# Optimization experiments

Measured on AMD Instinct MI355X. Metric: run time of the kernel, lower is better.

The kernel has to match this reference:

```python
import jax, jax.numpy as jnp
import numpy as np

N, E, H, L, R, NG = 8192, 131072, 256, 3, 128, 64
NUM_ELEMENTS = 80
CUTOFF = 12.0
INV_SQRT_2 = 1.0 / np.sqrt(2.0)
INV_SQRT_3 = 1.0 / np.sqrt(3.0)
INV_SQRT_H = 1.0 / np.sqrt(H)


def _glorot(key, shape):
    fan_in, fan_out = shape[-2], shape[-1]
    return jax.random.normal(key, shape, jnp.float32) * np.sqrt(2.0 / (fan_in + fan_out))


def setup_inputs():
    key = jax.random.key(0)
    ks = jax.random.split(key, 24)
    pos = jax.random.normal(ks[0], (N, 3), jnp.float32) * 5.0
    z = jax.random.randint(ks[1], (N,), 0, NUM_ELEMENTS)
    src = jax.random.randint(ks[2], (E,), 0, N)
    off = jax.random.randint(ks[3], (E,), 1, N)
    dst = (src + off) % N  # guarantee no self-loops (dist > 0)
    edge_index = jnp.stack([src, dst])
    batch = jnp.sort(jax.random.randint(ks[4], (N,), 0, NG))
    return {
        "pos": pos,
        "atom_emb": jax.random.normal(ks[5], (NUM_ELEMENTS, H), jnp.float32),
        "ln_w": jnp.ones((L, H), jnp.float32),
        "ln_b": jnp.zeros((L, H), jnp.float32),
        "xp_w1": _glorot(ks[6], (L, H, H)),
        "xp_b1": jnp.zeros((L, H), jnp.float32),
        "xp_w2": _glorot(ks[7], (L, H, 3 * H)),
        "xp_b2": jnp.zeros((L, 3 * H), jnp.float32),
        "rbf_w": _glorot(ks[8], (L, R, 3 * H)),
        "rbf_b": jnp.zeros((L, 3 * H), jnp.float32),
        "vec_w": _glorot(ks[9], (L, H, 2 * H)),
        "xv_w1": _glorot(ks[10], (L, 2 * H, H)),
        "xv_b1": jnp.zeros((L, H), jnp.float32),
        "xv_w2": _glorot(ks[11], (L, H, 3 * H)),
        "xv_b2": jnp.zeros((L, 3 * H), jnp.float32),
        "oe_w1": _glorot(ks[12], (H, H // 2)),
        "oe_b1": jnp.zeros((H // 2,), jnp.float32),
        "oe_w2": _glorot(ks[13], (H // 2, 1)),
        "oe_b2": jnp.zeros((1,), jnp.float32),
        "z": z,
        "edge_index": edge_index,
        "batch": batch,
    }


def _gaussian_rbf(dist):
    offset = jnp.linspace(0.0, CUTOFF, R)
    coeff = -0.5 / (offset[1] - offset[0]) ** 2
    return jnp.exp(coeff * (dist[:, None] - offset[None, :]) ** 2)  # [E, R]


def _layernorm(x, w, b):
    mu = x.mean(-1, keepdims=True)
    var = x.var(-1, keepdims=True)
    return (x - mu) / jnp.sqrt(var + 1e-5) * w + b


def reference(pos, atom_emb, ln_w, ln_b, xp_w1, xp_b1, xp_w2, xp_b2,
              rbf_w, rbf_b, vec_w, xv_w1, xv_b1, xv_w2, xv_b2,
              oe_w1, oe_b1, oe_w2, oe_b2, z, edge_index, batch):
    src, dst = edge_index[0], edge_index[1]
    rel = pos[src] - pos[dst]                       # [E, 3]
    dist = jnp.sqrt((rel ** 2).sum(-1))             # [E]
    edge_rbf = _gaussian_rbf(dist)                  # [E, R]
    edge_vector = rel / dist[:, None]               # [E, 3] unit vectors

    x = atom_emb[z]                                 # [N, H]
    vec = jnp.zeros((N, 3, H), x.dtype)

    for l in range(L):
        # ---- PaiNNMessage ----
        xh = _layernorm(x, ln_w[l], ln_b[l])
        xh = jax.nn.silu(xh @ xp_w1[l] + xp_b1[l]) @ xp_w2[l] + xp_b2[l]  # [N, 3H]
        rbfh = edge_rbf @ rbf_w[l] + rbf_b[l]                             # [E, 3H]
        m = xh[src] * rbfh
        mx, xh2, xh3 = jnp.split(m, 3, axis=-1)
        xh2 = xh2 * INV_SQRT_3
        mvec = (vec[src] * xh2[:, None, :] + xh3[:, None, :] * edge_vector[:, :, None]) * INV_SQRT_H
        dx = jax.ops.segment_sum(mx, dst, num_segments=N)
        dvec = jax.ops.segment_sum(mvec, dst, num_segments=N)
        x = (x + dx) * INV_SQRT_2
        vec = vec + dvec

        # ---- PaiNNUpdate ----
        vp = vec @ vec_w[l]                          # [N, 3, 2H]
        vec1, vec2 = jnp.split(vp, 2, axis=-1)
        vec_dot = (vec1 * vec2).sum(axis=1) * INV_SQRT_H           # [N, H]
        vnorm = jnp.sqrt((vec2 ** 2).sum(axis=1) + 1e-8)           # [N, H]
        h = jnp.concatenate([x, vnorm], axis=-1)
        h = jax.nn.silu(h @ xv_w1[l] + xv_b1[l]) @ xv_w2[l] + xv_b2[l]
        xv1, xv2, xv3 = jnp.split(h, 3, axis=-1)
        dx = (xv1 + xv2 * vec_dot) * INV_SQRT_2
        dvec = xv3[:, None, :] * vec1
        x = (x + dx) * INV_SQRT_2
        vec = vec + dvec

    # ---- energy head: per-atom MLP then per-molecule sum ----
    per_atom = jax.nn.silu(x @ oe_w1 + oe_b1) @ oe_w2 + oe_b2      # [N, 1]
    energy = jax.ops.segment_sum(per_atom, batch, num_segments=NG)  # [NG, 1]
    return energy
```

## Files before the change

### kernel.cpp

```cpp
#include <hip/hip_runtime.h>
#include <hip/hip_bf16.h>
#include <math.h>

#define NN 8192
#define EE 131072
#define HH 256
#define LL 3
#define RR 128
#define NGG 64
#define MSG_WAVES 16

typedef __attribute__((ext_vector_type(8))) short bf16x8;
typedef __attribute__((ext_vector_type(4))) float f32x4;
typedef unsigned short u16;

union U4 { ushort4 v; unsigned short a[4]; };
union U8 { uint4 v; unsigned short a[8]; };

__device__ __forceinline__ float silu(float v) { return v / (1.0f + expf(-v)); }
__device__ __forceinline__ float b2f(unsigned short u) { return __uint_as_float(((unsigned)u) << 16); }
__device__ __forceinline__ unsigned short f2b(float f) {
    unsigned u = __float_as_uint(f);
    u += 0x7fff + ((u >> 16) & 1);
    return (unsigned short)(u >> 16);
}

constexpr float kInvSqrt2 = 0.70710678118654752440f;
constexpr float kInvSqrt3 = 0.57735026918962576451f;
constexpr float kInvSqrtH = 0.0625f;

__global__ void k_zero(float* __restrict__ p, int n4) {
    int i = blockIdx.x * 256 + threadIdx.x;
    if (i < n4) ((float4*)p)[i] = make_float4(0.f, 0.f, 0.f, 0.f);
}

__global__ __launch_bounds__(256) void k_wt_all(
    const float* __restrict__ xp_w1, const float* __restrict__ xp_w2,
    const float* __restrict__ rbf_w, const float* __restrict__ vec_w,
    const float* __restrict__ xv_w1, const float* __restrict__ xv_w2,
    const float* __restrict__ oe_w1,
    u16* __restrict__ xp_w1T, u16* __restrict__ xp_w2T, u16* __restrict__ rbf_wKb,
    u16* __restrict__ vec_wT, u16* __restrict__ xv_w1T, u16* __restrict__ xv_w2T,
    u16* __restrict__ oe_w1T) {
    int bid = blockIdx.x;
    const float* src; u16* dst; int K, N, t, cast = 0;
    if (bid < 2400) {
        int l = bid / 800, r = bid % 800;
        if (r < 64)       { src = xp_w1 + (size_t)l * 65536;  dst = xp_w1T + (size_t)l * 65536;  K = 256; N = 256; t = r; }
        else if (r < 256) { src = xp_w2 + (size_t)l * 196608; dst = xp_w2T + (size_t)l * 196608; K = 256; N = 768; t = r - 64; }
        else if (r < 352) { src = rbf_w + (size_t)l * 98304;  dst = rbf_wKb + (size_t)l * 98304; K = 128; N = 768; t = r - 256; cast = 1; }
        else if (r < 480) { src = vec_w + (size_t)l * 131072; dst = vec_wT + (size_t)l * 131072; K = 256; N = 512; t = r - 352; }
        else if (r < 608) { src = xv_w1 + (size_t)l * 131072; dst = xv_w1T + (size_t)l * 131072; K = 512; N = 256; t = r - 480; }
        else              { src = xv_w2 + (size_t)l * 196608; dst = xv_w2T + (size_t)l * 196608; K = 256; N = 768; t = r - 608; }
    } else {
        src = oe_w1; dst = oe_w1T; K = 256; N = 128; t = bid - 2400;
    }
    int nx = N >> 5;
    int bn = (t % nx) * 32, bk = (t / nx) * 32;
    int tx = threadIdx.x & 31, ty = threadIdx.x >> 5;
    if (cast) {
#pragma unroll
        for (int i = 0; i < 32; i += 8)
            dst[(size_t)(bk + ty + i) * N + bn + tx] = f2b(src[(size_t)(bk + ty + i) * N + bn + tx]);
        return;
    }
    __shared__ float tile[32][33];
#pragma unroll
    for (int i = 0; i < 32; i += 8)
        tile[ty + i][tx] = src[(size_t)(bk + ty + i) * N + bn + tx];
    __syncthreads();
#pragma unroll
    for (int i = 0; i < 32; i += 8)
        dst[(size_t)(bn + ty + i) * K + bk + tx] = f2b(tile[tx][ty + i]);
}

__global__ void k_init_ln(const float* __restrict__ emb, const int* __restrict__ z,
                          const float* __restrict__ w, const float* __restrict__ b,
                          float* __restrict__ x, u16* __restrict__ xlnb) {
    int n = blockIdx.x, t = threadIdx.x;
    float v = emb[z[n] * HH + t];
    x[(size_t)n * HH + t] = v;
    float s = v, q = v * v;
#pragma unroll
    for (int m = 32; m >= 1; m >>= 1) {
        s += __shfl_xor(s, m, 64);
        q += __shfl_xor(q, m, 64);
    }
    __shared__ float s_sum[4], s_sq[4];
    int wid = t >> 6;
    if ((t & 63) == 0) { s_sum[wid] = s; s_sq[wid] = q; }
    __syncthreads();
    float S = s_sum[0] + s_sum[1] + s_sum[2] + s_sum[3];
    float Q = s_sq[0] + s_sq[1] + s_sq[2] + s_sq[3];
    float mu = S * (1.0f / HH);
    float var = Q * (1.0f / HH) - mu * mu;
    float rs = rsqrtf(var + 1e-5f);
    xlnb[(size_t)n * HH + t] = f2b((v - mu) * rs * w[t] + b[t]);
}

__global__ void k_geom_hist(const float* __restrict__ pos, const int* __restrict__ ei,
                            float* __restrict__ ev, int* __restrict__ deg) {
    int e = blockIdx.x * 256 + threadIdx.x;
    if (e >= EE) return;
    int s = ei[e], d = ei[EE + e];
    float rx = pos[s * 3 + 0] - pos[d * 3 + 0];
    float ry = pos[s * 3 + 1] - pos[d * 3 + 1];
    float rz = pos[s * 3 + 2] - pos[d * 3 + 2];
    float dist = sqrtf(rx * rx + ry * ry + rz * rz);
    float inv = 1.0f / dist;
    ((float4*)ev)[e] = make_float4(rx * inv, ry * inv, rz * inv, dist);
    atomicAdd(&deg[d], 1);
}

__global__ void k_scan_sort(const int* __restrict__ deg, int* __restrict__ row_ptr,
                            int* __restrict__ fill, int* __restrict__ dorder) {
    __shared__ int buf[256];
    __shared__ int carry_s;
    int t = threadIdx.x;
    if (t == 0) carry_s = 0;
    __syncthreads();
    for (int r = 0; r < NN; r += 256) {
        int v = deg[r + t];
        buf[t] = v;
        __syncthreads();
        for (int ofs = 1; ofs < 256; ofs <<= 1) {
            int add = (t >= ofs) ? buf[t - ofs] : 0;
            __syncthreads();
            buf[t] += add;
            __syncthreads();
        }
        int excl = buf[t] - v;
        int carry = carry_s;
        row_ptr[r + t] = carry + excl;
        fill[r + t] = carry + excl;
        __syncthreads();
        if (t == 255) carry_s = carry + buf[t];
        __syncthreads();
    }
    if (t == 0) row_ptr[NN] = carry_s;
    __syncthreads();
    __shared__ int bins[256];
    __shared__ int base[256];
    bins[t] = 0;
    __syncthreads();
    for (int d = t; d < NN; d += 256) {
        int b = deg[d]; b = b > 255 ? 255 : b;
        atomicAdd(&bins[b], 1);
    }
    __syncthreads();
    if (t == 0) {
        int acc = 0;
        for (int k = 255; k >= 0; --k) { base[k] = acc; acc += bins[k]; }
    }
    __syncthreads();
    bins[t] = 0;
    __syncthreads();
    for (int d = t; d < NN; d += 256) {
        int b = deg[d]; b = b > 255 ? 255 : b;
        int p = atomicAdd(&bins[b], 1);
        dorder[base[b] + p] = d;
    }
}

__global__ void k_scatter(const int* __restrict__ ei, const float* __restrict__ ev,
                          int* __restrict__ fill, int* __restrict__ srcp,
                          float4* __restrict__ evp, int* __restrict__ k0tab,
                          float* __restrict__ gtab) {
    int e = blockIdx.x * 256 + threadIdx.x;
    if (e >= EE) return;
    int d = ei[EE + e];
    int pos = atomicAdd(&fill[d], 1);
    float4 e4 = ((const float4*)ev)[e];
    srcp[pos] = ei[e];
    evp[pos] = e4;
    const float step = 12.0f / 127.0f;
    const float coeff = -0.5f / (step * step);
    float dist = e4.w;
    int k0 = (int)floorf(dist / step) - 3;
    k0 = k0 < 0 ? 0 : (k0 > 120 ? 120 : k0);
    float g[8];
#pragma unroll
    for (int k = 0; k < 8; ++k) {
        float t = dist - (k0 + k) * step;
        g[k] = expf(coeff * t * t);
    }
    k0tab[pos] = k0;
    ((float4*)gtab)[pos * 2 + 0] = make_float4(g[0], g[1], g[2], g[3]);
    ((float4*)gtab)[pos * 2 + 1] = make_float4(g[4], g[5], g[6], g[7]);
}

template <int AF32, int OUT_BF16, int ACT>
__global__ __launch_bounds__(256) void k_gemm(
    const void* __restrict__ Av, const u16* __restrict__ BT,
    const float* __restrict__ bias, void* __restrict__ C, int M, int K, int N) {
    __shared__ uint4 As4[512];
    __shared__ uint4 Bs4[512];
    u16* As = (u16*)As4;
    u16* Bs = (u16*)Bs4;
    int tid = threadIdx.x;
    int wave = tid >> 6, lane = tid & 63;
    int bm = blockIdx.y * 128, bn = blockIdx.x * 128;
    int wm = (wave >> 1) * 64, wn = (wave & 1) * 64;
    int lm = lane & 15;
    int kg = lane >> 4;
    f32x4 acc[4][4] = {};

    for (int k0 = 0; k0 < K; k0 += 32) {
#pragma unroll
        for (int it = 0; it < 2; ++it) {
            int idx = it * 256 + tid;
            int r = idx >> 2, seg = idx & 3;
            if (AF32) {
                const float* Af = (const float*)Av;
                float4 fa = *(const float4*)&Af[(size_t)(bm + r) * K + k0 + seg * 8];
                float4 fb = *(const float4*)&Af[(size_t)(bm + r) * K + k0 + seg * 8 + 4];
                U8 u;
                u.a[0] = f2b(fa.x); u.a[1] = f2b(fa.y); u.a[2] = f2b(fa.z); u.a[3] = f2b(fa.w);
                u.a[4] = f2b(fb.x); u.a[5] = f2b(fb.y); u.a[6] = f2b(fb.z); u.a[7] = f2b(fb.w);
                As4[idx] = u.v;
            } else {
                const u16* A = (const u16*)Av;
                As4[idx] = *(const uint4*)&A[(size_t)(bm + r) * K + k0 + seg * 8];
            }
            Bs4[idx] = *(const uint4*)&BT[(size_t)(bn + r) * K + k0 + seg * 8];
        }
        __syncthreads();
        bf16x8 af[4], bfr[4];
#pragma unroll
        for (int i = 0; i < 4; ++i)
            af[i] = *(const bf16x8*)&As[(wm + i * 16 + lm) * 32 + kg * 8];
#pragma unroll
        for (int j = 0; j < 4; ++j)
            bfr[j] = *(const bf16x8*)&Bs[(wn + j * 16 + lm) * 32 + kg * 8];
#pragma unroll
        for (int i = 0; i < 4; ++i)
#pragma unroll
            for (int j = 0; j < 4; ++j)
                acc[i][j] = __builtin_amdgcn_mfma_f32_16x16x32_bf16(af[i], bfr[j], acc[i][j], 0, 0, 0);
        __syncthreads();
    }

#pragma unroll
    for (int j = 0; j < 4; ++j) {
        int col = bn + wn + j * 16 + lm;
        float bv = bias ? bias[col] : 0.f;
#pragma unroll
        for (int i = 0; i < 4; ++i) {
            int row0 = bm + wm + i * 16 + kg * 4;
#pragma unroll
            for (int r = 0; r < 4; ++r) {
                float v = acc[i][j][r] + bv;
                if (ACT) v = silu(v);
                if (OUT_BF16)
                    ((u16*)C)[(size_t)(row0 + r) * N + col] = f2b(v);
                else
                    ((float*)C)[(size_t)(row0 + r) * N + col] = v;
            }
        }
    }
}

__global__ __launch_bounds__(1024) void k_msg(
    const u16* __restrict__ xhb, const u16* __restrict__ vinb,
    const int* __restrict__ srcp, const float4* __restrict__ evp,
    const int* __restrict__ row_ptr, const int* __restrict__ k0tab,
    const float* __restrict__ gtab, const u16* __restrict__ WK ,
    const float* __restrict__ rbias, float* __restrict__ x,
    const float* __restrict__ vin, float* __restrict__ vecM,
    const int* __restrict__ dorder) {
    __shared__ u16 Wp[128 * 256];
    int tid = threadIdx.x;
    int wave = tid >> 6, lane = tid & 63;
    int c0 = lane * 4;
    int blk = blockIdx.x;
    int band = (blk < 256) ? blk : (767 - blk);
    int d = dorder[band * MSG_WAVES + wave];
    int E0 = row_ptr[d], E1 = row_ptr[d + 1];
    float accv[3][4] = {};

#pragma unroll
    for (int p = 0; p < 3; ++p) {
        __syncthreads();
#pragma unroll
        for (int it = 0; it < 4; ++it) {
            int idx = it * 1024 + tid;
            int row = idx >> 5;
            int col8 = (idx & 31) * 8;
            *(uint4*)&Wp[row * 256 + col8] =
                *(const uint4*)&WK[(size_t)row * 768 + p * 256 + col8];
        }
        __syncthreads();
        float4 bb = ((const float4*)(rbias + p * 256))[lane];
        float bias4[4] = {bb.x, bb.y, bb.z, bb.w};
        float accx[4] = {};
        for (int j = E0; j < E1; ++j) {
            int s = srcp[j];
            int kj = k0tab[j];
            float4 ga = ((const float4*)gtab)[(size_t)j * 2 + 0];
            float4 gb = ((const float4*)gtab)[(size_t)j * 2 + 1];
            float g[8] = {ga.x, ga.y, ga.z, ga.w, gb.x, gb.y, gb.z, gb.w};
            float rr[4] = {bias4[0], bias4[1], bias4[2], bias4[3]};
#pragma unroll
            for (int k = 0; k < 8; ++k) {
                U4 w;
                w.v = *(const ushort4*)&Wp[(kj + k) * 256 + c0];
#pragma unroll
                for (int c = 0; c < 4; ++c) rr[c] += g[k] * b2f(w.a[c]);
            }
            if (p == 0) {
                U4 X; X.v = *(const ushort4*)(xhb + (size_t)s * 768 + c0);
#pragma unroll
                for (int c = 0; c < 4; ++c) accx[c] += b2f(X.a[c]) * rr[c];
            } else if (p == 1) {
                U4 X, V0, V1, V2;
                X.v = *(const ushort4*)(xhb + (size_t)s * 768 + 256 + c0);
                V0.v = *(const ushort4*)(vinb + (size_t)s * 768 + c0);
                V1.v = *(const ushort4*)(vinb + (size_t)s * 768 + 256 + c0);
                V2.v = *(const ushort4*)(vinb + (size_t)s * 768 + 512 + c0);
#pragma unroll
                for (int c = 0; c < 4; ++c) {
                    float m1 = b2f(X.a[c]) * rr[c] * kInvSqrt3;
                    accv[0][c] += b2f(V0.a[c]) * m1;
                    accv[1][c] += b2f(V1.a[c]) * m1;
                    accv[2][c] += b2f(V2.a[c]) * m1;
                }
            } else {
                U4 X; X.v = *(const ushort4*)(xhb + (size_t)s * 768 + 512 + c0);
                float4 ev4 = evp[j];
#pragma unroll
                for (int c = 0; c < 4; ++c) {
                    float m2 = b2f(X.a[c]) * rr[c];
                    accv[0][c] += m2 * ev4.x;
                    accv[1][c] += m2 * ev4.y;
                    accv[2][c] += m2 * ev4.z;
                }
            }
        }
        if (p == 0) {
            size_t xi = (size_t)d * 256 + c0;
            float4 xv = *(const float4*)&x[xi];
            xv.x = (xv.x + accx[0]) * kInvSqrt2;
            xv.y = (xv.y + accx[1]) * kInvSqrt2;
            xv.z = (xv.z + accx[2]) * kInvSqrt2;
            xv.w = (xv.w + accx[3]) * kInvSqrt2;
            *(float4*)&x[xi] = xv;
        }
    }
#pragma unroll
    for (int k = 0; k < 3; ++k) {
        size_t idx = (size_t)d * 768 + k * 256 + c0;
        float4 vv = *(const float4*)&vin[idx];
        vv.x += accv[k][0] * kInvSqrtH;
        vv.y += accv[k][1] * kInvSqrtH;
        vv.z += accv[k][2] * kInvSqrtH;
        vv.w += accv[k][3] * kInvSqrtH;
        *(float4*)&vecM[idx] = vv;
    }
}

__global__ void k_vecdot(const u16* __restrict__ vp, const float* __restrict__ x,
                         float* __restrict__ vec_dot, u16* __restrict__ hcat) {
    int i = blockIdx.x * 256 + threadIdx.x;
    int n = i >> 8, c = i & 255;
    const u16* p = vp + (size_t)n * 1536;
    float dsum = 0.f, qsum = 0.f;
#pragma unroll
    for (int k = 0; k < 3; ++k) {
        float v1 = b2f(p[k * 512 + c]);
        float v2 = b2f(p[k * 512 + 256 + c]);
        dsum += v1 * v2;
        qsum += v2 * v2;
    }
    vec_dot[i] = dsum * kInvSqrtH;
    hcat[(size_t)n * 512 + c] = f2b(x[i]);
    hcat[(size_t)n * 512 + 256 + c] = f2b(sqrtf(qsum + 1e-8f));
}

__global__ void k_update_out(const u16* __restrict__ hout, const float* __restrict__ vec_dot,
                             const u16* __restrict__ vp, float* __restrict__ x,
                             const float* __restrict__ vecM, float* __restrict__ vfin,
                             u16* __restrict__ vb,
                             const float* __restrict__ lnw, const float* __restrict__ lnb,
                             u16* __restrict__ xout) {
    int n = blockIdx.x, t = threadIdx.x;
    size_t i = (size_t)n * 256 + t;
    float xv1 = b2f(hout[(size_t)n * 768 + t]);
    float xv2 = b2f(hout[(size_t)n * 768 + 256 + t]);
    float xv3 = b2f(hout[(size_t)n * 768 + 512 + t]);
    float dxv = (xv1 + xv2 * vec_dot[i]) * kInvSqrt2;
    float nx = (x[i] + dxv) * kInvSqrt2;
    x[i] = nx;
#pragma unroll
    for (int k = 0; k < 3; ++k) {
        size_t idx = (size_t)n * 768 + k * 256 + t;
        float nv = vecM[idx] + xv3 * b2f(vp[(size_t)n * 1536 + k * 512 + t]);
        vfin[idx] = nv;
        vb[idx] = f2b(nv);
    }
    if (lnw) {
        float s = nx, q = nx * nx;
#pragma unroll
        for (int m = 32; m >= 1; m >>= 1) {
            s += __shfl_xor(s, m, 64);
            q += __shfl_xor(q, m, 64);
        }
        __shared__ float s_sum[4], s_sq[4];
        int wid = t >> 6;
        if ((t & 63) == 0) { s_sum[wid] = s; s_sq[wid] = q; }
        __syncthreads();
        float S = s_sum[0] + s_sum[1] + s_sum[2] + s_sum[3];
        float Q = s_sq[0] + s_sq[1] + s_sq[2] + s_sq[3];
        float mu = S * (1.0f / HH);
        float var = Q * (1.0f / HH) - mu * mu;
        float rs = rsqrtf(var + 1e-5f);
        xout[i] = f2b((nx - mu) * rs * lnw[t] + lnb[t]);
    } else {
        xout[i] = f2b(nx);
    }
}

__global__ void k_energy2(const float* __restrict__ h, const float* __restrict__ w2,
                          const float* __restrict__ b2, const int* __restrict__ batch,
                          float* __restrict__ out) {
    __shared__ float g[NGG];
    int t = threadIdx.x;
    if (t < NGG) g[t] = 0.f;
    __syncthreads();
    int a = blockIdx.x * 256 + t;
    const float4* hr = (const float4*)(h + (size_t)a * 128);
    const float4* w4 = (const float4*)w2;
    float acc = 0.f;
#pragma unroll 8
    for (int i = 0; i < 32; ++i) {
        float4 hv = hr[i], wv = w4[i];
        acc += hv.x * wv.x + hv.y * wv.y + hv.z * wv.z + hv.w * wv.w;
    }
    acc += b2[0];
    atomicAdd(&g[batch[a]], acc);
    __syncthreads();
    if (t < NGG && g[t] != 0.f) atomicAdd(&out[t], g[t]);
}

extern "C" void kernel_launch(void* const* d_in, const int* in_sizes, int n_in,
                              void* d_out, int out_size, void* d_ws, size_t ws_size,
                              hipStream_t stream) {
    const float* pos      = (const float*)d_in[0];
    const float* atom_emb = (const float*)d_in[1];
    const float* ln_w     = (const float*)d_in[2];
    const float* ln_b     = (const float*)d_in[3];
    const float* xp_w1    = (const float*)d_in[4];
    const float* xp_b1    = (const float*)d_in[5];
    const float* xp_w2    = (const float*)d_in[6];
    const float* xp_b2    = (const float*)d_in[7];
    const float* rbf_w    = (const float*)d_in[8];
    const float* rbf_b    = (const float*)d_in[9];
    const float* vec_w    = (const float*)d_in[10];
    const float* xv_w1    = (const float*)d_in[11];
    const float* xv_b1    = (const float*)d_in[12];
    const float* xv_w2    = (const float*)d_in[13];
    const float* xv_b2    = (const float*)d_in[14];
    const float* oe_w1    = (const float*)d_in[15];
    const float* oe_b1    = (const float*)d_in[16];
    const float* oe_w2    = (const float*)d_in[17];
    const float* oe_b2    = (const float*)d_in[18];
    const int*   z        = (const int*)d_in[19];
    const int*   ei       = (const int*)d_in[20];
    const int*   batch    = (const int*)d_in[21];
    float* out = (float*)d_out;

    char* ws = (char*)d_ws;
    size_t off = 0;
    auto alloc = [&](size_t b) {
        void* p = ws + off;
        off = (off + b + 255) & ~(size_t)255;
        return p;
    };
    float*  x      = (float*)alloc((size_t)NN * HH * 4);
    float*  vecA   = (float*)alloc((size_t)NN * 768 * 4);
    u16*    vb     = (u16*)alloc((size_t)NN * 768 * 2);
    float*  vecM   = (float*)alloc((size_t)NN * 768 * 4);
    u16*    xlnb   = (u16*)alloc((size_t)NN * HH * 2);
    u16*    t1b    = (u16*)alloc((size_t)NN * HH * 2);
    u16*    xhb    = (u16*)alloc((size_t)NN * 768 * 2);
    float*  vdot   = (float*)alloc((size_t)NN * HH * 4);
    u16*    vpb    = (u16*)alloc((size_t)NN * 1536 * 2);
    u16*    houtb  = (u16*)alloc((size_t)NN * 768 * 2);
    float*  ev     = (float*)alloc((size_t)EE * 4 * 4);
    int*    deg    = (int*)alloc((size_t)NN * 4);
    int*    row_ptr= (int*)alloc((size_t)(NN + 1) * 4);
    int*    fill   = (int*)alloc((size_t)NN * 4);
    int*    dorder = (int*)alloc((size_t)NN * 4);
    int*    srcp   = (int*)alloc((size_t)EE * 4);
    float4* evp    = (float4*)alloc((size_t)EE * 16);
    int*    k0tab  = (int*)alloc((size_t)EE * 4);
    float*  gtab   = (float*)alloc((size_t)EE * 8 * 4);
    u16* xp_w1T   = (u16*)alloc((size_t)3 * 256 * 256 * 2);
    u16* xp_w2T   = (u16*)alloc((size_t)3 * 768 * 256 * 2);
    u16* rbf_wKb  = (u16*)alloc((size_t)3 * 128 * 768 * 2);
    u16* vec_wT   = (u16*)alloc((size_t)3 * 512 * 256 * 2);
    u16* xv_w1T   = (u16*)alloc((size_t)3 * 256 * 512 * 2);
    u16* xv_w2T   = (u16*)alloc((size_t)3 * 768 * 256 * 2);
    u16* oe_w1T   = (u16*)alloc((size_t)128 * 256 * 2);
    (void)ws_size;

    u16*   h1b   = t1b;
    u16*   hcatb = xhb;
    float* heng  = vdot;
    u16*   xb    = xlnb;

    k_wt_all<<<2432, 256, 0, stream>>>(xp_w1, xp_w2, rbf_w, vec_w, xv_w1, xv_w2, oe_w1,
                                       xp_w1T, xp_w2T, rbf_wKb, vec_wT, xv_w1T, xv_w2T, oe_w1T);
    k_zero<<<(36 * 1024 * 1024 / 16 + 255) / 256, 256, 0, stream>>>(vecA, 36 * 1024 * 1024 / 16);
    k_zero<<<8, 256, 0, stream>>>((float*)deg, NN / 4);
    k_init_ln<<<NN, 256, 0, stream>>>(atom_emb, z, ln_w, ln_b, x, xlnb);
    k_geom_hist<<<EE / 256, 256, 0, stream>>>(pos, ei, ev, deg);
    k_scan_sort<<<1, 256, 0, stream>>>(deg, row_ptr, fill, dorder);
    k_scatter<<<EE / 256, 256, 0, stream>>>(ei, ev, fill, srcp, evp, k0tab, gtab);

    for (int l = 0; l < LL; ++l) {
        k_gemm<0, 1, 1><<<dim3(2, NN / 128), 256, 0, stream>>>(
            xlnb, xp_w1T + (size_t)l * 256 * 256, xp_b1 + l * HH, t1b, NN, 256, 256);
        k_gemm<0, 1, 0><<<dim3(6, NN / 128), 256, 0, stream>>>(
            t1b, xp_w2T + (size_t)l * 768 * 256, xp_b2 + l * 768, xhb, NN, 256, 768);
        k_msg<<<NN / MSG_WAVES, 1024, 0, stream>>>(
            xhb, vb, srcp, evp, row_ptr, k0tab, gtab,
            rbf_wKb + (size_t)l * 128 * 768, rbf_b + l * 768, x, vecA, vecM, dorder);

        k_gemm<1, 1, 0><<<dim3(4, 3 * NN / 128), 256, 0, stream>>>(
            vecM, vec_wT + (size_t)l * 512 * 256, nullptr, vpb, 3 * NN, 256, 512);
        k_vecdot<<<NN, 256, 0, stream>>>(vpb, x, vdot, hcatb);
        k_gemm<0, 1, 1><<<dim3(2, NN / 128), 256, 0, stream>>>(
            hcatb, xv_w1T + (size_t)l * 256 * 512, xv_b1 + l * HH, h1b, NN, 512, 256);
        k_gemm<0, 1, 0><<<dim3(6, NN / 128), 256, 0, stream>>>(
            h1b, xv_w2T + (size_t)l * 768 * 256, xv_b2 + l * 768, houtb, NN, 256, 768);
        bool last = (l == LL - 1);
        k_update_out<<<NN, 256, 0, stream>>>(
            houtb, vdot, vpb, x, vecM, vecA, vb,
            last ? nullptr : ln_w + (l + 1) * HH,
            last ? nullptr : ln_b + (l + 1) * HH, xlnb);
    }

    k_gemm<0, 0, 1><<<dim3(1, NN / 128), 256, 0, stream>>>(
        xb, oe_w1T, oe_b1, heng, NN, 256, 128);
    k_zero<<<1, 256, 0, stream>>>(out, NGG / 4);
    k_energy2<<<32, 256, 0, stream>>>(heng, oe_w2, oe_b2, batch, out);
}
```

Baseline: 817.9 us.

## Pack RBF weights and gaussians as bf16 pairs and use fdot2 in message kernel

Measured after the change: 802.7 us. Within noise of the previous version (-1.9%).

```diff
diff --git a/kernel.cpp b/kernel.cpp
--- a/kernel.cpp
+++ b/kernel.cpp
@@ -14,8 +14,16 @@
 typedef __attribute__((ext_vector_type(4))) float f32x4;
 typedef unsigned short u16;
 
+#if defined(__has_builtin)
+#if __has_builtin(__builtin_amdgcn_fdot2_f32_bf16)
+#define HAVE_FDOT2 1
+typedef __attribute__((ext_vector_type(2))) __bf16 bf16x2_t;
+union BU { unsigned u; bf16x2_t v; };
+#endif
+#endif
+
 union U4 { ushort4 v; unsigned short a[4]; };
-union U8 { uint4 v; unsigned short a[8]; };
+union U8 { uint4 v; unsigned short a[8]; unsigned w[4]; };
 
 __device__ __forceinline__ float silu(float v) { return v / (1.0f + expf(-v)); }
 __device__ __forceinline__ float b2f(unsigned short u) { return __uint_as_float(((unsigned)u) << 16); }
@@ -39,16 +47,16 @@
     const float* __restrict__ rbf_w, const float* __restrict__ vec_w,
     const float* __restrict__ xv_w1, const float* __restrict__ xv_w2,
     const float* __restrict__ oe_w1,
-    u16* __restrict__ xp_w1T, u16* __restrict__ xp_w2T, u16* __restrict__ rbf_wKb,
+    u16* __restrict__ xp_w1T, u16* __restrict__ xp_w2T, u16* __restrict__ rbf_wP,
     u16* __restrict__ vec_wT, u16* __restrict__ xv_w1T, u16* __restrict__ xv_w2T,
     u16* __restrict__ oe_w1T) {
     int bid = blockIdx.x;
-    const float* src; u16* dst; int K, N, t, cast = 0;
+    const float* src; u16* dst; int K, N, t, pairmode = 0;
     if (bid < 2400) {
         int l = bid / 800, r = bid % 800;
         if (r < 64)       { src = xp_w1 + (size_t)l * 65536;  dst = xp_w1T + (size_t)l * 65536;  K = 256; N = 256; t = r; }
         else if (r < 256) { src = xp_w2 + (size_t)l * 196608; dst = xp_w2T + (size_t)l * 196608; K = 256; N = 768; t = r - 64; }
-        else if (r < 352) { src = rbf_w + (size_t)l * 98304;  dst = rbf_wKb + (size_t)l * 98304; K = 128; N = 768; t = r - 256; cast = 1; }
+        else if (r < 352) { src = rbf_w + (size_t)l * 98304;  dst = rbf_wP + (size_t)l * 98304;  K = 128; N = 768; t = r - 256; pairmode = 1; }
         else if (r < 480) { src = vec_w + (size_t)l * 131072; dst = vec_wT + (size_t)l * 131072; K = 256; N = 512; t = r - 352; }
         else if (r < 608) { src = xv_w1 + (size_t)l * 131072; dst = xv_w1T + (size_t)l * 131072; K = 512; N = 256; t = r - 480; }
         else              { src = xv_w2 + (size_t)l * 196608; dst = xv_w2T + (size_t)l * 196608; K = 256; N = 768; t = r - 608; }
@@ -58,10 +66,12 @@
     int nx = N >> 5;
     int bn = (t % nx) * 32, bk = (t / nx) * 32;
     int tx = threadIdx.x & 31, ty = threadIdx.x >> 5;
-    if (cast) {
-#pragma unroll
-        for (int i = 0; i < 32; i += 8)
-            dst[(size_t)(bk + ty + i) * N + bn + tx] = f2b(src[(size_t)(bk + ty + i) * N + bn + tx]);
+    if (pairmode) {
+#pragma unroll
+        for (int i = 0; i < 32; i += 8) {
+            int k = bk + ty + i, n = bn + tx;
+            dst[(size_t)(k >> 1) * 1536 + n * 2 + (k & 1)] = f2b(src[(size_t)k * N + n]);
+        }
         return;
     }
     __shared__ float tile[32][33];
@@ -164,8 +174,8 @@
 
 __global__ void k_scatter(const int* __restrict__ ei, const float* __restrict__ ev,
                           int* __restrict__ fill, int* __restrict__ srcp,
-                          float4* __restrict__ evp, int* __restrict__ k0tab,
-                          float* __restrict__ gtab) {
+                          float4* __restrict__ evp, int* __restrict__ kptab,
+                          unsigned* __restrict__ gtab) {
     int e = blockIdx.x * 256 + threadIdx.x;
     if (e >= EE) return;
     int d = ei[EE + e];
@@ -176,7 +186,7 @@
     const float step = 12.0f / 127.0f;
     const float coeff = -0.5f / (step * step);
     float dist = e4.w;
-    int k0 = (int)floorf(dist / step) - 3;
+    int k0 = ((int)floorf(dist / step) - 3) & ~1;
     k0 = k0 < 0 ? 0 : (k0 > 120 ? 120 : k0);
     float g[8];
 #pragma unroll
@@ -184,9 +194,12 @@
         float t = dist - (k0 + k) * step;
         g[k] = expf(coeff * t * t);
     }
-    k0tab[pos] = k0;
-    ((float4*)gtab)[pos * 2 + 0] = make_float4(g[0], g[1], g[2], g[3]);
-    ((float4*)gtab)[pos * 2 + 1] = make_float4(g[4], g[5], g[6], g[7]);
+    kptab[pos] = k0 >> 1;
+    unsigned g0 = (unsigned)f2b(g[0]) | ((unsigned)f2b(g[1]) << 16);
+    unsigned g1 = (unsigned)f2b(g[2]) | ((unsigned)f2b(g[3]) << 16);
+    unsigned g2 = (unsigned)f2b(g[4]) | ((unsigned)f2b(g[5]) << 16);
+    unsigned g3 = (unsigned)f2b(g[6]) | ((unsigned)f2b(g[7]) << 16);
+    ((uint4*)gtab)[pos] = make_uint4(g0, g1, g2, g3);
 }
 
 template <int AF32, int OUT_BF16, int ACT>
@@ -263,18 +276,16 @@
 __global__ __launch_bounds__(1024) void k_msg(
     const u16* __restrict__ xhb, const u16* __restrict__ vinb,
     const int* __restrict__ srcp, const float4* __restrict__ evp,
-    const int* __restrict__ row_ptr, const int* __restrict__ k0tab,
-    const float* __restrict__ gtab, const u16* __restrict__ WK ,
+    const int* __restrict__ row_ptr, const int* __restrict__ kptab,
+    const unsigned* __restrict__ gtab, const u16* __restrict__ WP ,
     const float* __restrict__ rbias, float* __restrict__ x,
     const float* __restrict__ vin, float* __restrict__ vecM,
     const int* __restrict__ dorder) {
-    __shared__ u16 Wp[128 * 256];
+    __shared__ u16 Wp[64 * 512];
     int tid = threadIdx.x;
     int wave = tid >> 6, lane = tid & 63;
     int c0 = lane * 4;
-    int blk = blockIdx.x;
-    int band = (blk < 256) ? blk : (767 - blk);
-    int d = dorder[band * MSG_WAVES + wave];
+    int d = dorder[blockIdx.x * MSG_WAVES + wave];
     int E0 = row_ptr[d], E1 = row_ptr[d + 1];
     float accv[3][4] = {};
 
@@ -284,10 +295,10 @@
 #pragma unroll
         for (int it = 0; it < 4; ++it) {
             int idx = it * 1024 + tid;
-            int row = idx >> 5;
-            int col8 = (idx & 31) * 8;
-            *(uint4*)&Wp[row * 256 + col8] =
-                *(const uint4*)&WK[(size_t)row * 768 + p * 256 + col8];
+            int r = idx >> 6;
+            int c8 = (idx & 63) * 8;
+            *(uint4*)&Wp[r * 512 + c8] =
+                *(const uint4*)&WP[(size_t)r * 1536 + p * 512 + c8];
         }
         __syncthreads();
         float4 bb = ((const float4*)(rbias + p * 256))[lane];
@@ -295,17 +306,28 @@
         float accx[4] = {};
         for (int j = E0; j < E1; ++j) {
             int s = srcp[j];
-            int kj = k0tab[j];
-            float4 ga = ((const float4*)gtab)[(size_t)j * 2 + 0];
-            float4 gb = ((const float4*)gtab)[(size_t)j * 2 + 1];
-            float g[8] = {ga.x, ga.y, ga.z, ga.w, gb.x, gb.y, gb.z, gb.w};
+            int kp = kptab[j];
+            uint4 gt = ((const uint4*)gtab)[j];
+            unsigned gp[4] = {gt.x, gt.y, gt.z, gt.w};
             float rr[4] = {bias4[0], bias4[1], bias4[2], bias4[3]};
 #pragma unroll
-            for (int k = 0; k < 8; ++k) {
-                U4 w;
-                w.v = *(const ushort4*)&Wp[(kj + k) * 256 + c0];
-#pragma unroll
-                for (int c = 0; c < 4; ++c) rr[c] += g[k] * b2f(w.a[c]);
+            for (int p2 = 0; p2 < 4; ++p2) {
+                U8 w;
+                w.v = *(const uint4*)&Wp[(kp + p2) * 512 + c0 * 2];
+#ifdef HAVE_FDOT2
+                BU gv; gv.u = gp[p2];
+#pragma unroll
+                for (int c = 0; c < 4; ++c) {
+                    BU wv; wv.u = w.w[c];
+                    rr[c] = __builtin_amdgcn_fdot2_f32_bf16(wv.v, gv.v, rr[c], false);
+                }
+#else
+                float ge = b2f((u16)(gp[p2] & 0xffff));
+                float go = b2f((u16)(gp[p2] >> 16));
+#pragma unroll
+                for (int c = 0; c < 4; ++c)
+                    rr[c] += ge * b2f(w.a[2 * c]) + go * b2f(w.a[2 * c + 1]);
+#endif
             }
             if (p == 0) {
                 U4 X; X.v = *(const ushort4*)(xhb + (size_t)s * 768 + c0);
@@ -475,28 +497,28 @@
         off = (off + b + 255) & ~(size_t)255;
         return p;
     };
-    float*  x      = (float*)alloc((size_t)NN * HH * 4);
-    float*  vecA   = (float*)alloc((size_t)NN * 768 * 4);
-    u16*    vb     = (u16*)alloc((size_t)NN * 768 * 2);
-    float*  vecM   = (float*)alloc((size_t)NN * 768 * 4);
-    u16*    xlnb   = (u16*)alloc((size_t)NN * HH * 2);
-    u16*    t1b    = (u16*)alloc((size_t)NN * HH * 2);
-    u16*    xhb    = (u16*)alloc((size_t)NN * 768 * 2);
-    float*  vdot   = (float*)alloc((size_t)NN * HH * 4);
-    u16*    vpb    = (u16*)alloc((size_t)NN * 1536 * 2);
-    u16*    houtb  = (u16*)alloc((size_t)NN * 768 * 2);
-    float*  ev     = (float*)alloc((size_t)EE * 4 * 4);
-    int*    deg    = (int*)alloc((size_t)NN * 4);
-    int*    row_ptr= (int*)alloc((size_t)(NN + 1) * 4);
-    int*    fill   = (int*)alloc((size_t)NN * 4);
-    int*    dorder = (int*)alloc((size_t)NN * 4);
-    int*    srcp   = (int*)alloc((size_t)EE * 4);
-    float4* evp    = (float4*)alloc((size_t)EE * 16);
-    int*    k0tab  = (int*)alloc((size_t)EE * 4);
-    float*  gtab   = (float*)alloc((size_t)EE * 8 * 4);
+    float*    x      = (float*)alloc((size_t)NN * HH * 4);
+    float*    vecA   = (float*)alloc((size_t)NN * 768 * 4);
+    u16*      vb     = (u16*)alloc((size_t)NN * 768 * 2);
+    float*    vecM   = (float*)alloc((size_t)NN * 768 * 4);
+    u16*      xlnb   = (u16*)alloc((size_t)NN * HH * 2);
+    u16*      t1b    = (u16*)alloc((size_t)NN * HH * 2);
+    u16*      xhb    = (u16*)alloc((size_t)NN * 768 * 2);
+    float*    vdot   = (float*)alloc((size_t)NN * HH * 4);
+    u16*      vpb    = (u16*)alloc((size_t)NN * 1536 * 2);
+    u16*      houtb  = (u16*)alloc((size_t)NN * 768 * 2);
+    float*    ev     = (float*)alloc((size_t)EE * 4 * 4);
+    int*      deg    = (int*)alloc((size_t)NN * 4);
+    int*      row_ptr= (int*)alloc((size_t)(NN + 1) * 4);
+    int*      fill   = (int*)alloc((size_t)NN * 4);
+    int*      dorder = (int*)alloc((size_t)NN * 4);
+    int*      srcp   = (int*)alloc((size_t)EE * 4);
+    float4*   evp    = (float4*)alloc((size_t)EE * 16);
+    int*      kptab  = (int*)alloc((size_t)EE * 4);
+    unsigned* gtab   = (unsigned*)alloc((size_t)EE * 16);
     u16* xp_w1T   = (u16*)alloc((size_t)3 * 256 * 256 * 2);
     u16* xp_w2T   = (u16*)alloc((size_t)3 * 768 * 256 * 2);
-    u16* rbf_wKb  = (u16*)alloc((size_t)3 * 128 * 768 * 2);
+    u16* rbf_wP   = (u16*)alloc((size_t)3 * 128 * 768 * 2);
     u16* vec_wT   = (u16*)alloc((size_t)3 * 512 * 256 * 2);
     u16* xv_w1T   = (u16*)alloc((size_t)3 * 256 * 512 * 2);
     u16* xv_w2T   = (u16*)alloc((size_t)3 * 768 * 256 * 2);
@@ -509,13 +531,13 @@
     u16*   xb    = xlnb;
 
     k_wt_all<<<2432, 256, 0, stream>>>(xp_w1, xp_w2, rbf_w, vec_w, xv_w1, xv_w2, oe_w1,
-                                       xp_w1T, xp_w2T, rbf_wKb, vec_wT, xv_w1T, xv_w2T, oe_w1T);
+                                       xp_w1T, xp_w2T, rbf_wP, vec_wT, xv_w1T, xv_w2T, oe_w1T);
     k_zero<<<(36 * 1024 * 1024 / 16 + 255) / 256, 256, 0, stream>>>(vecA, 36 * 1024 * 1024 / 16);
     k_zero<<<8, 256, 0, stream>>>((float*)deg, NN / 4);
     k_init_ln<<<NN, 256, 0, stream>>>(atom_emb, z, ln_w, ln_b, x, xlnb);
     k_geom_hist<<<EE / 256, 256, 0, stream>>>(pos, ei, ev, deg);
     k_scan_sort<<<1, 256, 0, stream>>>(deg, row_ptr, fill, dorder);
-    k_scatter<<<EE / 256, 256, 0, stream>>>(ei, ev, fill, srcp, evp, k0tab, gtab);
+    k_scatter<<<EE / 256, 256, 0, stream>>>(ei, ev, fill, srcp, evp, kptab, gtab);
 
     for (int l = 0; l < LL; ++l) {
         k_gemm<0, 1, 1><<<dim3(2, NN / 128), 256, 0, stream>>>(
@@ -523,8 +545,8 @@
         k_gemm<0, 1, 0><<<dim3(6, NN / 128), 256, 0, stream>>>(
             t1b, xp_w2T + (size_t)l * 768 * 256, xp_b2 + l * 768, xhb, NN, 256, 768);
         k_msg<<<NN / MSG_WAVES, 1024, 0, stream>>>(
-            xhb, vb, srcp, evp, row_ptr, k0tab, gtab,
-            rbf_wKb + (size_t)l * 128 * 768, rbf_b + l * 768, x, vecA, vecM, dorder);
+            xhb, vb, srcp, evp, row_ptr, kptab, gtab,
+            rbf_wP + (size_t)l * 128 * 768, rbf_b + l * 768, x, vecA, vecM, dorder);
 
         k_gemm<1, 1, 0><<<dim3(4, 3 * NN / 128), 256, 0, stream>>>(
             vecM, vec_wT + (size_t)l * 512 * 256, nullptr, vpb, 3 * NN, 256, 512);
```
